# Kernel optimization log

Measured on AMD Instinct MI355X. Metric: run time of the kernel, lower is better.

## Reference

```python
import jax, jax.numpy as jnp
import numpy as np

B, E, C, K, H, OUT = 8192, 16, 256, 2, 64, 387

def setup_inputs() -> dict:
    ks = jax.random.split(jax.random.key(0), 6)
    x = jax.random.normal(ks[0], (B, E, C), dtype=jnp.float32)
    adj = jax.random.normal(ks[1], (E, E), dtype=jnp.float32) * (6.0 / (E + E)) ** 0.5  # xavier-ish
    adj_bias = jax.random.normal(ks[2], (1,), dtype=jnp.float32) * 0.1
    cheb_w = jax.random.normal(ks[3], (K * C, H), dtype=jnp.float32) * (6.0 / (K * C + H)) ** 0.5
    brelu_bias = jnp.zeros((1, 1, H), dtype=jnp.float32)
    fc_w = jax.random.normal(ks[4], (OUT, H), dtype=jnp.float32) * (1.0 / H) ** 0.5
    fc_b = jax.random.normal(ks[5], (OUT,), dtype=jnp.float32) * (1.0 / H) ** 0.5
    return {"x": x, "adj": adj, "adj_bias": adj_bias, "cheb_w": cheb_w,
            "brelu_bias": brelu_bias, "fc_w": fc_w, "fc_b": fc_b}

def reference(x, adj, adj_bias, cheb_w, brelu_bias, fc_w, fc_b):
    # adaptive adjacency + biased ReLU (Eq. 4 prelude)
    w = jax.nn.relu(adj + adj_bias)  # (E,E)
    # normalized Laplacian: I - D^{-1/2} W D^{-1/2}
    d_re = 1.0 / jnp.sqrt(jnp.sum(w, axis=1) + 1e-5)  # (E,)
    lap = jnp.eye(E, dtype=x.dtype) - d_re[:, None] * w * d_re[None, :]  # (E,E)
    # Chebyshev polynomial, k=2: T0 = ones, T1 = lap @ x
    t0 = jnp.ones_like(x)                       # (B,E,C)
    t1 = jnp.einsum('ij,bjc->bic', lap, x)      # (B,E,C)
    # torch: stack on dim=1 -> permute(0,2,3,1) -> flatten(2)  == interleave along last axis
    cp = jnp.stack([t0, t1], axis=-1).reshape(B, E, K * C)  # (B,E,K*C)
    h = jnp.einsum('bek,kh->beh', cp, cheb_w)   # (B,E,H)
    # dropout is identity at eval
    h = jax.nn.relu(brelu_bias + h)
    out = jnp.einsum('beh,oh->beo', h, fc_w) + fc_b  # (B,E,OUT)
    return out
```

## Files before the change

kernel.cpp:

```cpp
#include <hip/hip_runtime.h>
#include <stdint.h>


typedef __attribute__((ext_vector_type(4))) float f32x4;
typedef __attribute__((ext_vector_type(8))) short s16x8;
typedef __attribute__((ext_vector_type(4))) short s16x4;

#define WS_CH_B    0
#define WS_LAP_B   256
#define WS_LAPA_B  1280
#define WS_W1T_B   2048
#define WS_FCW_B   34816
#define FCW_ROWS   400

static __device__ __forceinline__ short f2bf(float f) {
    union { float f; uint32_t u; } v; v.f = f;
    uint32_t r = (v.u + 0x7fffu + ((v.u >> 16) & 1u)) >> 16;
    return (short)r;
}

__global__ void prep_kernel(const float* __restrict__ adj,
                            const float* __restrict__ adj_bias,
                            const float* __restrict__ cheb_w,
                            const float* __restrict__ brelu_bias,
                            const float* __restrict__ fc_w,
                            char* __restrict__ ws) {
    float* chf  = (float*)(ws + WS_CH_B);
    float* lapf = (float*)(ws + WS_LAP_B);
    short* lapA = (short*)(ws + WS_LAPA_B);
    short* w1t  = (short*)(ws + WS_W1T_B);
    short* fcw  = (short*)(ws + WS_FCW_B);
    int t = threadIdx.x;

    if (blockIdx.x == 0) {
        __shared__ float sw[16][17];
        __shared__ float sdre[16];
        __shared__ float slap[16][16];
        float ab = adj_bias[0];
        {
            int i = t >> 4, j = t & 15;
            sw[i][j] = fmaxf(adj[t] + ab, 0.f);
        }
        __syncthreads();
        if (t < 16) {
            float s = 0.f;
            #pragma unroll
            for (int j = 0; j < 16; ++j) s += sw[t][j];
            sdre[t] = 1.0f / sqrtf(s + 1e-5f);
        }
        __syncthreads();
        {
            int i = t >> 4, j = t & 15;
            float l = (i == j ? 1.f : 0.f) - sdre[i] * sw[i][j] * sdre[j];
            slap[i][j] = l;
            lapf[t] = l;
        }
        __syncthreads();
        if (t < 64) {
            int m = t & 15, q = t >> 4;
            #pragma unroll
            for (int i = 0; i < 4; ++i)
                lapA[t * 4 + i] = f2bf(slap[m][q * 4 + i]);
            float s = 0.f;
            for (int c = 0; c < 256; ++c) s += cheb_w[(2 * c) * 64 + t];
            chf[t] = s + brelu_bias[t];
        }
    }
    int gt = blockIdx.x * blockDim.x + t;
    int nthr = gridDim.x * blockDim.x;
    for (int idx = gt; idx < 64 * 256; idx += nthr) {
        int hh = idx >> 8, c = idx & 255;
        w1t[idx] = f2bf(cheb_w[(2 * c + 1) * 64 + hh]);
    }
    for (int idx = gt; idx < FCW_ROWS * 64; idx += nthr) {
        fcw[idx] = (idx < 387 * 64) ? f2bf(fc_w[idx]) : (short)0;
    }
}

__global__ __launch_bounds__(256) void fused_kernel(
        const float* __restrict__ x,
        const float* __restrict__ fc_b,
        const char* __restrict__ ws,
        float* __restrict__ out) {
    const float* chf  = (const float*)(ws + WS_CH_B);
    const short* lapA = (const short*)(ws + WS_LAPA_B);
    const short* w1t  = (const short*)(ws + WS_W1T_B);
    const short* fcw  = (const short*)(ws + WS_FCW_B);

    __shared__ __align__(16) short hs[4][16][72];

    const int lane = threadIdx.x & 63;
    const int wave = threadIdx.x >> 6;
    const int n = lane & 15;
    const int q = lane >> 4;
    const long b = (long)blockIdx.x * 4 + wave;

    const float* xb = x + b * 4096;

    f32x4 g[4];
    #pragma unroll
    for (int nt = 0; nt < 4; ++nt) g[nt] = (f32x4){0.f, 0.f, 0.f, 0.f};
    #pragma unroll
    for (int kb = 0; kb < 8; ++kb) {
        const int k0 = kb * 32 + q * 8;
        const f32x4* xp = (const f32x4*)(xb + n * 256 + k0);
        f32x4 xa = xp[0], xc = xp[1];
        s16x8 af;
        af[0] = f2bf(xa[0]); af[1] = f2bf(xa[1]); af[2] = f2bf(xa[2]); af[3] = f2bf(xa[3]);
        af[4] = f2bf(xc[0]); af[5] = f2bf(xc[1]); af[6] = f2bf(xc[2]); af[7] = f2bf(xc[3]);
        #pragma unroll
        for (int nt = 0; nt < 4; ++nt) {
            s16x8 bf = *(const s16x8*)(w1t + (nt * 16 + n) * 256 + k0);
            g[nt] = __builtin_amdgcn_mfma_f32_16x16x32_bf16(af, bf, g[nt], 0, 0, 0);
        }
    }

    f32x4 h[4];
#if defined(__has_builtin) && __has_builtin(__builtin_amdgcn_mfma_f32_16x16x16bf16_1k)
    {
        s16x4 la = *(const s16x4*)(lapA + lane * 4);
        const f32x4 z4 = (f32x4){0.f, 0.f, 0.f, 0.f};
        #pragma unroll
        for (int nt = 0; nt < 4; ++nt) {
            s16x4 gb;
            gb[0] = f2bf(g[nt][0]); gb[1] = f2bf(g[nt][1]);
            gb[2] = f2bf(g[nt][2]); gb[3] = f2bf(g[nt][3]);
            h[nt] = __builtin_amdgcn_mfma_f32_16x16x16bf16_1k(la, gb, z4, 0, 0, 0);
        }
    }
#else
    {
        __shared__ float gs[4][16][68];
        const float* lapf = (const float*)(ws + WS_LAP_B);
        #pragma unroll
        for (int r = 0; r < 4; ++r) {
            gs[wave][q * 4 + r][0 * 16 + n] = g[0][r];
            gs[wave][q * 4 + r][1 * 16 + n] = g[1][r];
            gs[wave][q * 4 + r][2 * 16 + n] = g[2][r];
            gs[wave][q * 4 + r][3 * 16 + n] = g[3][r];
        }
        __syncthreads();
        #pragma unroll
        for (int nt = 0; nt < 4; ++nt) h[nt] = (f32x4){0.f, 0.f, 0.f, 0.f};
        #pragma unroll
        for (int e = 0; e < 16; ++e) {
            float l0 = lapf[(q * 4 + 0) * 16 + e];
            float l1 = lapf[(q * 4 + 1) * 16 + e];
            float l2 = lapf[(q * 4 + 2) * 16 + e];
            float l3 = lapf[(q * 4 + 3) * 16 + e];
            #pragma unroll
            for (int nt = 0; nt < 4; ++nt) {
                float gv = gs[wave][e][nt * 16 + n];
                h[nt][0] += l0 * gv; h[nt][1] += l1 * gv;
                h[nt][2] += l2 * gv; h[nt][3] += l3 * gv;
            }
        }
    }
#endif

    #pragma unroll
    for (int nt = 0; nt < 4; ++nt) {
        float cv = chf[nt * 16 + n];
        #pragma unroll
        for (int r = 0; r < 4; ++r) {
            float v = fmaxf(h[nt][r] + cv, 0.f);
            hs[wave][q * 4 + r][nt * 16 + n] = f2bf(v);
        }
    }
    __syncthreads();

    s16x8 ha0 = *(const s16x8*)(&hs[wave][n][q * 8]);
    s16x8 ha1 = *(const s16x8*)(&hs[wave][n][32 + q * 8]);
    float* outb = out + (b * 16 + q * 4) * 387;
    for (int tt = 0; tt < 25; ++tt) {
        const int o0 = tt * 16;
        s16x8 fb0 = *(const s16x8*)(fcw + (o0 + n) * 64 + q * 8);
        s16x8 fb1 = *(const s16x8*)(fcw + (o0 + n) * 64 + 32 + q * 8);
        f32x4 acc = (f32x4){0.f, 0.f, 0.f, 0.f};
        acc = __builtin_amdgcn_mfma_f32_16x16x32_bf16(ha0, fb0, acc, 0, 0, 0);
        acc = __builtin_amdgcn_mfma_f32_16x16x32_bf16(ha1, fb1, acc, 0, 0, 0);
        const int o = o0 + n;
        if (o < 387) {
            float bias = fc_b[o];
            outb[0 * 387 + o] = acc[0] + bias;
            outb[1 * 387 + o] = acc[1] + bias;
            outb[2 * 387 + o] = acc[2] + bias;
            outb[3 * 387 + o] = acc[3] + bias;
        }
    }
}

extern "C" void kernel_launch(void* const* d_in, const int* in_sizes, int n_in,
                              void* d_out, int out_size, void* d_ws, size_t ws_size,
                              hipStream_t stream) {
    const float* x          = (const float*)d_in[0];
    const float* adj        = (const float*)d_in[1];
    const float* adj_bias   = (const float*)d_in[2];
    const float* cheb_w     = (const float*)d_in[3];
    const float* brelu_bias = (const float*)d_in[4];
    const float* fc_w       = (const float*)d_in[5];
    const float* fc_b       = (const float*)d_in[6];
    float* outp = (float*)d_out;
    char* ws = (char*)d_ws;

    prep_kernel<<<32, 256, 0, stream>>>(adj, adj_bias, cheb_w, brelu_bias, fc_w, ws);
    fused_kernel<<<2048, 256, 0, stream>>>(x, fc_b, ws, outp);
}
```

Measured before the change: 376.9 us.

## Prefetch all x loads upfront, fold fc bias into accumulator, parallelize prep sums

The fused kernel now issues all 16 vector loads of the x row before any conversion or MFMA, so more memory requests are in flight per wave. The fc bias is padded into the workspace and used as the MFMA accumulator's initial value, which removes the per-output adds, and the output loop is fully unrolled. The prep kernel splits the cheb_w column sums across all 256 threads, runs 64 blocks instead of 32, and fused_kernel gets a launch-bounds occupancy hint. The extra live registers from the prefetched x could pressure occupancy.

New measurement: 389.1 us. +3.2%, slower.

```diff
diff --git a/kernel.cpp b/kernel.cpp
--- a/kernel.cpp
+++ b/kernel.cpp
@@ -9,8 +9,9 @@
 #define WS_CH_B    0
 #define WS_LAP_B   256
 #define WS_LAPA_B  1280
-#define WS_W1T_B   2048
-#define WS_FCW_B   34816
+#define WS_FCB_B   1792
+#define WS_W1T_B   4096
+#define WS_FCW_B   36864
 #define FCW_ROWS   400
 
 static __device__ __forceinline__ short f2bf(float f) {
@@ -24,10 +25,12 @@
                             const float* __restrict__ cheb_w,
                             const float* __restrict__ brelu_bias,
                             const float* __restrict__ fc_w,
+                            const float* __restrict__ fc_b,
                             char* __restrict__ ws) {
     float* chf  = (float*)(ws + WS_CH_B);
     float* lapf = (float*)(ws + WS_LAP_B);
     short* lapA = (short*)(ws + WS_LAPA_B);
+    float* fcbp = (float*)(ws + WS_FCB_B);
     short* w1t  = (short*)(ws + WS_W1T_B);
     short* fcw  = (short*)(ws + WS_FCW_B);
     int t = threadIdx.x;
@@ -36,10 +39,18 @@
         __shared__ float sw[16][17];
         __shared__ float sdre[16];
         __shared__ float slap[16][16];
+        __shared__ float csum[4][64];
         float ab = adj_bias[0];
         {
             int i = t >> 4, j = t & 15;
             sw[i][j] = fmaxf(adj[t] + ab, 0.f);
+        }
+        {
+            int hh = t & 63, part = t >> 6;
+            float s = 0.f;
+            #pragma unroll 8
+            for (int i = 0; i < 64; ++i) s += cheb_w[(2 * (part * 64 + i)) * 64 + hh];
+            csum[part][hh] = s;
         }
         __syncthreads();
         if (t < 16) {
@@ -57,14 +68,13 @@
         }
         __syncthreads();
         if (t < 64) {
-            int m = t & 15, q = t >> 4;
+            int m = t & 15, qq = t >> 4;
             #pragma unroll
             for (int i = 0; i < 4; ++i)
-                lapA[t * 4 + i] = f2bf(slap[m][q * 4 + i]);
-            float s = 0.f;
-            for (int c = 0; c < 256; ++c) s += cheb_w[(2 * c) * 64 + t];
-            chf[t] = s + brelu_bias[t];
-        }
+                lapA[t * 4 + i] = f2bf(slap[m][qq * 4 + i]);
+            chf[t] = csum[0][t] + csum[1][t] + csum[2][t] + csum[3][t] + brelu_bias[t];
+        }
+        for (int o = t; o < 400; o += 256) fcbp[o] = (o < 387) ? fc_b[o] : 0.f;
     }
     int gt = blockIdx.x * blockDim.x + t;
     int nthr = gridDim.x * blockDim.x;
@@ -77,13 +87,13 @@
     }
 }
 
-__global__ __launch_bounds__(256) void fused_kernel(
+__global__ __launch_bounds__(256, 4) void fused_kernel(
         const float* __restrict__ x,
-        const float* __restrict__ fc_b,
         const char* __restrict__ ws,
         float* __restrict__ out) {
     const float* chf  = (const float*)(ws + WS_CH_B);
     const short* lapA = (const short*)(ws + WS_LAPA_B);
+    const float* fcbp = (const float*)(ws + WS_FCB_B);
     const short* w1t  = (const short*)(ws + WS_W1T_B);
     const short* fcw  = (const short*)(ws + WS_FCW_B);
 
@@ -97,21 +107,32 @@
 
     const float* xb = x + b * 4096;
 
+    const float* xrow = xb + n * 256 + q * 8;
+    f32x4 xr[16];
+    #pragma unroll
+    for (int kb = 0; kb < 8; ++kb) {
+        xr[2 * kb]     = *(const f32x4*)(xrow + kb * 32);
+        xr[2 * kb + 1] = *(const f32x4*)(xrow + kb * 32 + 4);
+    }
+    s16x8 af[8];
+    #pragma unroll
+    for (int kb = 0; kb < 8; ++kb) {
+        f32x4 xa = xr[2 * kb], xc = xr[2 * kb + 1];
+        af[kb][0] = f2bf(xa[0]); af[kb][1] = f2bf(xa[1]);
+        af[kb][2] = f2bf(xa[2]); af[kb][3] = f2bf(xa[3]);
+        af[kb][4] = f2bf(xc[0]); af[kb][5] = f2bf(xc[1]);
+        af[kb][6] = f2bf(xc[2]); af[kb][7] = f2bf(xc[3]);
+    }
     f32x4 g[4];
     #pragma unroll
     for (int nt = 0; nt < 4; ++nt) g[nt] = (f32x4){0.f, 0.f, 0.f, 0.f};
     #pragma unroll
     for (int kb = 0; kb < 8; ++kb) {
         const int k0 = kb * 32 + q * 8;
-        const f32x4* xp = (const f32x4*)(xb + n * 256 + k0);
-        f32x4 xa = xp[0], xc = xp[1];
-        s16x8 af;
-        af[0] = f2bf(xa[0]); af[1] = f2bf(xa[1]); af[2] = f2bf(xa[2]); af[3] = f2bf(xa[3]);
-        af[4] = f2bf(xc[0]); af[5] = f2bf(xc[1]); af[6] = f2bf(xc[2]); af[7] = f2bf(xc[3]);
         #pragma unroll
         for (int nt = 0; nt < 4; ++nt) {
             s16x8 bf = *(const s16x8*)(w1t + (nt * 16 + n) * 256 + k0);
-            g[nt] = __builtin_amdgcn_mfma_f32_16x16x32_bf16(af, bf, g[nt], 0, 0, 0);
+            g[nt] = __builtin_amdgcn_mfma_f32_16x16x32_bf16(af[kb], bf, g[nt], 0, 0, 0);
         }
     }
 
@@ -172,20 +193,21 @@
     s16x8 ha0 = *(const s16x8*)(&hs[wave][n][q * 8]);
     s16x8 ha1 = *(const s16x8*)(&hs[wave][n][32 + q * 8]);
     float* outb = out + (b * 16 + q * 4) * 387;
+    #pragma unroll
     for (int tt = 0; tt < 25; ++tt) {
         const int o0 = tt * 16;
         s16x8 fb0 = *(const s16x8*)(fcw + (o0 + n) * 64 + q * 8);
         s16x8 fb1 = *(const s16x8*)(fcw + (o0 + n) * 64 + 32 + q * 8);
-        f32x4 acc = (f32x4){0.f, 0.f, 0.f, 0.f};
+        const int o = o0 + n;
+        float bias = fcbp[o];
+        f32x4 acc = (f32x4){bias, bias, bias, bias};
         acc = __builtin_amdgcn_mfma_f32_16x16x32_bf16(ha0, fb0, acc, 0, 0, 0);
         acc = __builtin_amdgcn_mfma_f32_16x16x32_bf16(ha1, fb1, acc, 0, 0, 0);
-        const int o = o0 + n;
         if (o < 387) {
-            float bias = fc_b[o];
-            outb[0 * 387 + o] = acc[0] + bias;
-            outb[1 * 387 + o] = acc[1] + bias;
-            outb[2 * 387 + o] = acc[2] + bias;
-            outb[3 * 387 + o] = acc[3] + bias;
+            outb[0 * 387 + o] = acc[0];
+            outb[1 * 387 + o] = acc[1];
+            outb[2 * 387 + o] = acc[2];
+            outb[3 * 387 + o] = acc[3];
         }
     }
 }
@@ -203,6 +225,6 @@
     float* outp = (float*)d_out;
     char* ws = (char*)d_ws;
 
-    prep_kernel<<<32, 256, 0, stream>>>(adj, adj_bias, cheb_w, brelu_bias, fc_w, ws);
-    fused_kernel<<<2048, 256, 0, stream>>>(x, fc_b, ws, outp);
-}
+    prep_kernel<<<64, 256, 0, stream>>>(adj, adj_bias, cheb_w, brelu_bias, fc_w, fc_b, ws);
+    fused_kernel<<<2048, 256, 0, stream>>>(x, ws, outp);
+}
```
